# Optimization experiments

Measured on AMD Instinct MI355X. Metric: run time of the kernel, lower is better.

Reference implementation:

```python
import jax, jax.numpy as jnp
import numpy as np

B, S, D, H = 2, 4096, 512, 8
HD = D // H
SCALE = HD ** -0.5


def setup_inputs() -> dict:
    key = jax.random.key(0)
    ks = jax.random.split(key, 11)
    std = D ** -0.5
    return {
        "query": jax.random.normal(ks[0], (B, S, D), jnp.float32),
        "key":   jax.random.normal(ks[1], (B, S, D), jnp.float32),
        "value": jax.random.normal(ks[2], (B, S, D), jnp.float32),
        "wq": jax.random.normal(ks[3], (D, D), jnp.float32) * std,
        "bq": jnp.zeros((D,), jnp.float32),
        "wk": jax.random.normal(ks[4], (D, D), jnp.float32) * std,
        "bk": jnp.zeros((D,), jnp.float32),
        "wv": jax.random.normal(ks[5], (D, D), jnp.float32) * std,
        "bv": jnp.zeros((D,), jnp.float32),
        "wo": jax.random.normal(ks[6], (D, D), jnp.float32) * std,
        "bo": jnp.zeros((D,), jnp.float32),
    }


def reference(query, key, value, wq, bq, wk, bk, wv, bv, wo, bo):
    # projections: [B,S,D] -> [B,H,S,HD]
    def split_heads(x):
        return x.reshape(B, S, H, HD).transpose(0, 2, 1, 3)

    q = split_heads(query @ wq + bq)
    k = split_heads(key @ wk + bk)
    v = split_heads(value @ wv + bv)

    # full O(S^2) score matrix, as in the original naive MHA
    scores = jnp.einsum("bhqd,bhkd->bhqk", q, k) * SCALE  # [B,H,S,S]
    attn_weights = jax.nn.softmax(scores, axis=-1)
    attn_output = jnp.einsum("bhqk,bhkd->bhqd", attn_weights, v)
    attn_output = attn_output.transpose(0, 2, 1, 3).reshape(B, S, D)
    attn_output = attn_output @ wo + bo
    return attn_output, attn_weights
```

## Files before the change

kernel.cpp:

```cpp
#include <hip/hip_runtime.h>
#include <hip/hip_bf16.h>
#include <cstdint>
#include <cstddef>

#define B_  2
#define S_  4096
#define D_  512
#define H_  8
#define HD_ 64
#define QSCALE_ 0.18033688f

typedef short s16x8 __attribute__((ext_vector_type(8)));
typedef float f32x4 __attribute__((ext_vector_type(4)));

__device__ __forceinline__ unsigned short f2bf(float f) {
    unsigned u = __builtin_bit_cast(unsigned, f);
    u += 0x7fffu + ((u >> 16) & 1u);
    return (unsigned short)(u >> 16);
}

__device__ __forceinline__ unsigned packbf2(float a, float b) {
    unsigned r;
    asm("v_cvt_pk_bf16_f32 %0, %1, %2" : "=v"(r) : "v"(a), "v"(b));
    return r;
}

__device__ __forceinline__ void gload16(const unsigned short* g, const unsigned short* l) {
    __builtin_amdgcn_global_load_lds(
        (const __attribute__((address_space(1))) void*)g,
        (__attribute__((address_space(3))) void*)l,
        16, 0, 0);
}

__device__ __forceinline__ s16x8 kfr(const unsigned short* buf, int kr, int hb) {
    return *(const s16x8*)((const char*)buf + kr * 128 + (hb ^ ((kr & 7) << 4)));
}
__device__ __forceinline__ s16x8 vfr_(const unsigned short* buf, int vr, int kbyte) {
    return *(const s16x8*)((const char*)buf + vr * 256 + (kbyte ^ ((vr & 15) << 4)));
}

__global__ __launch_bounds__(256)
void prep_weights(const float* __restrict__ wq, const float* __restrict__ wk,
                  const float* __restrict__ wv, const float* __restrict__ wo,
                  unsigned short* __restrict__ wt) {
    int e = blockIdx.x * 256 + threadIdx.x;
    int mat = e >> 18;
    int i = e & 262143;
    int n = i >> 9, k = i & 511;
    const float* w = (mat == 0) ? wq : (mat == 1) ? wk : (mat == 2) ? wv : wo;
    wt[(size_t)mat * 262144 + n * 512 + k] = f2bf(w[k * 512 + n]);
}

__global__ __launch_bounds__(256)
void qkv_gemm(const float* __restrict__ qx, const float* __restrict__ kx,
              const float* __restrict__ vx, const unsigned short* __restrict__ wtb,
              const float* __restrict__ bqp, const float* __restrict__ bkp,
              const float* __restrict__ bvp,
              unsigned short* __restrict__ qo, unsigned short* __restrict__ ko,
              unsigned short* __restrict__ vo) {
    __shared__ unsigned short xs[64 * 72];
    __shared__ unsigned short wsd[64 * 72];

    const int z = blockIdx.z;
    const float* xin = (z == 0) ? qx : (z == 1) ? kx : vx;
    const unsigned short* wt = wtb + (size_t)z * 262144;
    const float* bias = (z == 0) ? bqp : (z == 1) ? bkp : bvp;
    const float oscale = (z == 0) ? QSCALE_ : 1.0f;

    const int tid  = threadIdx.x;
    const int wave = tid >> 6, lane = tid & 63;
    const int l15 = lane & 15, l4 = lane >> 4;
    const int row0 = blockIdx.x * 64, col0 = blockIdx.y * 64;
    const int sr = tid >> 2, seg = tid & 3;

    f32x4 acc[4] = {};

    for (int kt = 0; kt < 512; kt += 64) {
        {
            const float* x = xin + (size_t)(row0 + sr) * 512 + kt + seg * 16;
            unsigned short tmp[16];
            #pragma unroll
            for (int j = 0; j < 16; j += 4) {
                float4 v = *(const float4*)(x + j);
                tmp[j] = f2bf(v.x); tmp[j+1] = f2bf(v.y); tmp[j+2] = f2bf(v.z); tmp[j+3] = f2bf(v.w);
            }
            *(s16x8*)&xs[sr * 72 + seg * 16]     = *(s16x8*)&tmp[0];
            *(s16x8*)&xs[sr * 72 + seg * 16 + 8] = *(s16x8*)&tmp[8];
        }
        {
            const unsigned short* wp = wt + (size_t)(col0 + sr) * 512 + kt + seg * 16;
            *(s16x8*)&wsd[sr * 72 + seg * 16]     = *(const s16x8*)(wp);
            *(s16x8*)&wsd[sr * 72 + seg * 16 + 8] = *(const s16x8*)(wp + 8);
        }
        __syncthreads();

        #pragma unroll
        for (int ks = 0; ks < 2; ++ks) {
            s16x8 a = *(const s16x8*)&xs[(wave * 16 + l15) * 72 + ks * 32 + l4 * 8];
            #pragma unroll
            for (int ng = 0; ng < 4; ++ng) {
                s16x8 b = *(const s16x8*)&wsd[(ng * 16 + l15) * 72 + ks * 32 + l4 * 8];
                acc[ng] = __builtin_amdgcn_mfma_f32_16x16x32_bf16(a, b, acc[ng], 0, 0, 0);
            }
        }
        __syncthreads();
    }

    if (z == 2) {
        #pragma unroll
        for (int ng = 0; ng < 4; ++ng) {
            float bv = bias[col0 + ng * 16 + l15];
            #pragma unroll
            for (int r = 0; r < 4; ++r)
                xs[(ng * 16 + l15) * 72 + wave * 16 + l4 * 4 + r] = f2bf(acc[ng][r] + bv);
        }
        __syncthreads();
        const int bb = row0 >> 12, s0l = row0 & 4095, hh = col0 >> 6;
        unsigned short* dst = vo + ((size_t)(bb * H_ + hh) * HD_ + sr) * S_ + s0l + seg * 16;
        *(s16x8*)dst       = *(const s16x8*)&xs[sr * 72 + seg * 16];
        *(s16x8*)(dst + 8) = *(const s16x8*)&xs[sr * 72 + seg * 16 + 8];
    } else {
        unsigned short* out = (z == 0) ? qo : ko;
        #pragma unroll
        for (int ng = 0; ng < 4; ++ng) {
            int c = col0 + ng * 16 + l15;
            float bv = bias[c];
            #pragma unroll
            for (int r = 0; r < 4; ++r) {
                int t = row0 + wave * 16 + l4 * 4 + r;
                out[(size_t)t * 512 + c] = f2bf((acc[ng][r] + bv) * oscale);
            }
        }
    }
}

__global__ __launch_bounds__(256)
void oproj_gemm(const unsigned short* __restrict__ xin, const unsigned short* __restrict__ wt,
                const float* __restrict__ bias, float* __restrict__ out) {
    __shared__ unsigned short xs[64 * 72];
    __shared__ unsigned short wsd[64 * 72];

    const int tid  = threadIdx.x;
    const int wave = tid >> 6, lane = tid & 63;
    const int l15 = lane & 15, l4 = lane >> 4;
    const int row0 = blockIdx.x * 64, col0 = blockIdx.y * 64;
    const int sr = tid >> 2, seg = tid & 3;

    f32x4 acc[4] = {};

    for (int kt = 0; kt < 512; kt += 64) {
        {
            const unsigned short* x = xin + (size_t)(row0 + sr) * 512 + kt + seg * 16;
            *(s16x8*)&xs[sr * 72 + seg * 16]     = *(const s16x8*)(x);
            *(s16x8*)&xs[sr * 72 + seg * 16 + 8] = *(const s16x8*)(x + 8);
        }
        {
            const unsigned short* wp = wt + (size_t)(col0 + sr) * 512 + kt + seg * 16;
            *(s16x8*)&wsd[sr * 72 + seg * 16]     = *(const s16x8*)(wp);
            *(s16x8*)&wsd[sr * 72 + seg * 16 + 8] = *(const s16x8*)(wp + 8);
        }
        __syncthreads();

        #pragma unroll
        for (int ks = 0; ks < 2; ++ks) {
            s16x8 a = *(const s16x8*)&xs[(wave * 16 + l15) * 72 + ks * 32 + l4 * 8];
            #pragma unroll
            for (int ng = 0; ng < 4; ++ng) {
                s16x8 b = *(const s16x8*)&wsd[(ng * 16 + l15) * 72 + ks * 32 + l4 * 8];
                acc[ng] = __builtin_amdgcn_mfma_f32_16x16x32_bf16(a, b, acc[ng], 0, 0, 0);
            }
        }
        __syncthreads();
    }

    #pragma unroll
    for (int ng = 0; ng < 4; ++ng) {
        int c = col0 + ng * 16 + l15;
        float bv = bias[c];
        #pragma unroll
        for (int r = 0; r < 4; ++r) {
            int t = row0 + wave * 16 + l4 * 4 + r;
            out[(size_t)t * 512 + c] = acc[ng][r] + bv;
        }
    }
}

__global__ __launch_bounds__(256)
void attn_kernel(const unsigned short* __restrict__ qb,
                 const unsigned short* __restrict__ kb,
                 const unsigned short* __restrict__ vt,
                 float* __restrict__ wout,
                 unsigned short* __restrict__ ob) {
    __shared__ unsigned short smem[40960];

    const int tid  = threadIdx.x;
    const int wave = tid >> 6, lane = tid & 63;
    const int l15 = lane & 15, l4 = lane >> 4;

    const int lid = blockIdx.x;
    const int wid = (lid & 7) * 64 + (lid >> 3);
    const int bh = wid >> 5;
    const int q0 = (wid & 31) * 128;
    const int b = bh >> 3, h = bh & 7;

    const int ksrow = lane >> 3;
    const int kscol = 8 * ((lane & 7) ^ ksrow);
    const unsigned short* kstg0 = kb + (size_t)(b * S_ + wave * 32 + ksrow) * 512 + h * 64 + kscol;
    const unsigned short* kstg1 = kb + (size_t)(b * S_ + wave * 64 + ksrow) * 512 + h * 64 + kscol;
    const int vsrow = lane >> 4;

#define KSTAGE1(c, bsel)                                                        \
    { _Pragma("unroll")                                                         \
      for (int i_ = 0; i_ < 8; ++i_)                                            \
          gload16(kstg1 + ((size_t)(c) * 256 + i_ * 8) * 512,                   \
                  smem + (bsel) * 16384 + (wave * 64 + i_ * 8) * 64); }

#define KSTAGE(c, bsel)                                                         \
    { _Pragma("unroll")                                                         \
      for (int i_ = 0; i_ < 4; ++i_)                                            \
          gload16(kstg0 + ((size_t)(c) * 128 + i_ * 8) * 512,                   \
                  smem + (bsel) * 8192 + (wave * 32 + i_ * 8) * 64); }

#define VSTAGE(c, bsel)                                                         \
    { _Pragma("unroll")                                                         \
      for (int i_ = 0; i_ < 4; ++i_) {                                          \
          int vrow_ = wave * 16 + i_ * 4 + vsrow;                               \
          int vcb_  = (lane & 15) ^ (i_ * 4 + vsrow);                           \
          gload16(vt + ((size_t)(bh * 64) + vrow_) * 4096 + (c) * 128 + vcb_ * 8, \
                  smem + 16384 + (bsel) * 8192 + (wave * 16 + i_ * 4) * 128); } }

    s16x8 aq[2][2];
    #pragma unroll
    for (int qh = 0; qh < 2; ++qh) {
        const int t = b * S_ + q0 + wave * 32 + qh * 16 + l15;
        const unsigned short* qp = qb + (size_t)t * 512 + h * 64;
        aq[qh][0] = *(const s16x8*)(qp + l4 * 8);
        aq[qh][1] = *(const s16x8*)(qp + 32 + l4 * 8);
    }

    float lsum[2] = {0.0f, 0.0f};
    KSTAGE1(0, 0);
    __syncthreads();

    for (int c = 0; c < 16; ++c) {
        const int cur = c & 1;
        if (c < 15) KSTAGE1(c + 1, cur ^ 1);
        const unsigned short* kcur = smem + cur * 16384;

        #pragma unroll
        for (int sub = 0; sub < 4; ++sub) {
            f32x4 sc[4][2] = {};
            __builtin_amdgcn_s_setprio(1);
            #pragma unroll
            for (int ks = 0; ks < 2; ++ks)
                #pragma unroll
                for (int kg = 0; kg < 4; ++kg) {
                    s16x8 kf = kfr(kcur, sub * 64 + kg * 16 + l15, ks * 64 + l4 * 16);
                    sc[kg][0] = __builtin_amdgcn_mfma_f32_16x16x32_bf16(kf, aq[0][ks], sc[kg][0], 0, 0, 0);
                    sc[kg][1] = __builtin_amdgcn_mfma_f32_16x16x32_bf16(kf, aq[1][ks], sc[kg][1], 0, 0, 0);
                }
            __builtin_amdgcn_s_setprio(0);
            #pragma unroll
            for (int kg = 0; kg < 4; ++kg)
                #pragma unroll
                for (int r = 0; r < 4; ++r) {
                    lsum[0] += __builtin_amdgcn_exp2f(sc[kg][0][r]);
                    lsum[1] += __builtin_amdgcn_exp2f(sc[kg][1][r]);
                }
        }
        __syncthreads();
    }

    #pragma unroll
    for (int qh = 0; qh < 2; ++qh) {
        lsum[qh] += __shfl_xor(lsum[qh], 16);
        lsum[qh] += __shfl_xor(lsum[qh], 32);
    }
    const float off[2] = { -__builtin_amdgcn_logf(lsum[0]),
                           -__builtin_amdgcn_logf(lsum[1]) };

    f32x4 ao[2][4] = {};
    float* wbase = wout + ((size_t)bh * S_ + q0 + wave * 32) * S_;
    unsigned short* strip = smem + 32768 + wave * 2048;

    KSTAGE(0, 0); VSTAGE(0, 0);
    __syncthreads();

    for (int c = 0; c < 32; ++c) {
        const int cur = c & 1;
        if (c < 31) { KSTAGE(c + 1, cur ^ 1); VSTAGE(c + 1, cur ^ 1); }
        const unsigned short* kcur = smem + cur * 8192;
        const unsigned short* vcur = smem + 16384 + cur * 8192;

        #pragma unroll
        for (int sub = 0; sub < 2; ++sub) {
            f32x4 sc[4][2] = {};
            __builtin_amdgcn_s_setprio(1);
            #pragma unroll
            for (int ks = 0; ks < 2; ++ks)
                #pragma unroll
                for (int kg = 0; kg < 4; ++kg) {
                    s16x8 kf = kfr(kcur, sub * 64 + kg * 16 + l15, ks * 64 + l4 * 16);
                    sc[kg][0] = __builtin_amdgcn_mfma_f32_16x16x32_bf16(kf, aq[0][ks], sc[kg][0], 0, 0, 0);
                    sc[kg][1] = __builtin_amdgcn_mfma_f32_16x16x32_bf16(kf, aq[1][ks], sc[kg][1], 0, 0, 0);
                }
            __builtin_amdgcn_s_setprio(0);

            #pragma unroll
            for (int qh = 0; qh < 2; ++qh) {
                float* wrow = wbase + (size_t)(qh * 16 + l15) * S_ + c * 128 + sub * 64;
                const int q = qh * 16 + l15;
                #pragma unroll
                for (int kg = 0; kg < 4; ++kg) {
                    f32x4 w;
                    #pragma unroll
                    for (int r = 0; r < 4; ++r)
                        w[r] = __builtin_amdgcn_exp2f(sc[kg][qh][r] + off[qh]);
                    *(f32x4*)(wrow + kg * 16 + l4 * 4) = w;
                    uint2 pk;
                    pk.x = packbf2(w[0], w[1]);
                    pk.y = packbf2(w[2], w[3]);
                    *(uint2*)((char*)strip + q * 128 + ((kg * 32 + l4 * 8) ^ ((q & 7) << 4))) = pk;
                }
            }

            __builtin_amdgcn_s_setprio(1);
            #pragma unroll
            for (int ks = 0; ks < 2; ++ks) {
                s16x8 pa0 = *(const s16x8*)((const char*)strip + l15 * 128
                               + ((ks * 64 + l4 * 16) ^ ((l15 & 7) << 4)));
                s16x8 pa1 = *(const s16x8*)((const char*)strip + (16 + l15) * 128
                               + ((ks * 64 + l4 * 16) ^ ((l15 & 7) << 4)));
                #pragma unroll
                for (int ng = 0; ng < 4; ++ng) {
                    s16x8 vf = vfr_(vcur, ng * 16 + l15, sub * 128 + ks * 64 + l4 * 16);
                    ao[0][ng] = __builtin_amdgcn_mfma_f32_16x16x32_bf16(pa0, vf, ao[0][ng], 0, 0, 0);
                    ao[1][ng] = __builtin_amdgcn_mfma_f32_16x16x32_bf16(pa1, vf, ao[1][ng], 0, 0, 0);
                }
            }
            __builtin_amdgcn_s_setprio(0);
        }
        __syncthreads();
    }

    #pragma unroll
    for (int qg = 0; qg < 2; ++qg)
        #pragma unroll
        for (int ng = 0; ng < 4; ++ng) {
            int hd = ng * 16 + l15;
            #pragma unroll
            for (int r = 0; r < 4; ++r) {
                int t = b * S_ + q0 + wave * 32 + qg * 16 + l4 * 4 + r;
                ob[(size_t)t * 512 + h * 64 + hd] = f2bf(ao[qg][ng][r]);
            }
        }
#undef KSTAGE1
#undef KSTAGE
#undef VSTAGE
}

extern "C" void kernel_launch(void* const* d_in, const int* in_sizes, int n_in,
                              void* d_out, int out_size, void* d_ws, size_t ws_size,
                              hipStream_t stream) {
    (void)in_sizes; (void)n_in; (void)out_size; (void)ws_size;

    const float* query = (const float*)d_in[0];
    const float* key_  = (const float*)d_in[1];
    const float* value = (const float*)d_in[2];
    const float* wq = (const float*)d_in[3];
    const float* bq = (const float*)d_in[4];
    const float* wk = (const float*)d_in[5];
    const float* bk = (const float*)d_in[6];
    const float* wv = (const float*)d_in[7];
    const float* bv = (const float*)d_in[8];
    const float* wo = (const float*)d_in[9];
    const float* bo = (const float*)d_in[10];
    float* out = (float*)d_out;

    char* ws = (char*)d_ws;
    unsigned short* wt = (unsigned short*)(ws);
    unsigned short* qb = (unsigned short*)(ws + 2097152);
    unsigned short* kb = (unsigned short*)(ws + 2097152 + 1 * 8388608);
    unsigned short* vt = (unsigned short*)(ws + 2097152 + 2 * 8388608);
    unsigned short* ob = (unsigned short*)(ws + 2097152 + 3 * 8388608);

    hipLaunchKernelGGL(prep_weights, dim3(4096), dim3(256), 0, stream, wq, wk, wv, wo, wt);

    hipLaunchKernelGGL(qkv_gemm, dim3(128, 8, 3), dim3(256), 0, stream,
                       query, key_, value, wt, bq, bk, bv, qb, kb, vt);

    hipLaunchKernelGGL(attn_kernel, dim3(512), dim3(256), 0, stream,
                       qb, kb, vt, out + 4194304, ob);

    hipLaunchKernelGGL(oproj_gemm, dim3(128, 8), dim3(256), 0, stream,
                       ob, wt + 3 * 262144, bo, out);
}
```

Baseline: 354.7 us.

## Enlarge QKV GEMM tiles to 128x128 with swizzled LDS and async B loads

The QKV projection GEMM moves from 64x64 to 128x128 output tiles, with each of the four waves computing a 64x64 sub-tile of 4x4 MFMA fragments. This raises operand reuse from shared memory and cuts redundant global reads of the activations and weights. Padded LDS rows become XOR-swizzled rows, and weight tiles are loaded with the gload16 direct-to-LDS helper. The V transpose epilogue gets wider vectorised stores. The trade-offs are more accumulator registers and fewer blocks (768 instead of 3072), which may lower occupancy. This kernel is also a small part of total time, which is dominated by attention.

```diff
diff --git a/kernel.cpp b/kernel.cpp
--- a/kernel.cpp
+++ b/kernel.cpp
@@ -58,8 +58,9 @@
               const float* __restrict__ bvp,
               unsigned short* __restrict__ qo, unsigned short* __restrict__ ko,
               unsigned short* __restrict__ vo) {
-    __shared__ unsigned short xs[64 * 72];
-    __shared__ unsigned short wsd[64 * 72];
+    __shared__ unsigned short smem[16384];
+    unsigned short* as_ = smem;
+    unsigned short* bs_ = smem + 8192;
 
     const int z = blockIdx.z;
     const float* xin = (z == 0) ? qx : (z == 1) ? kx : vx;
@@ -70,66 +71,89 @@
     const int tid  = threadIdx.x;
     const int wave = tid >> 6, lane = tid & 63;
     const int l15 = lane & 15, l4 = lane >> 4;
-    const int row0 = blockIdx.x * 64, col0 = blockIdx.y * 64;
-    const int sr = tid >> 2, seg = tid & 3;
-
-    f32x4 acc[4] = {};
+    const int wr = wave >> 1, wc = wave & 1;
+    const int row0 = blockIdx.x * 128, col0 = blockIdx.y * 128;
+
+    const int arow = tid >> 1, ahalf = tid & 1;
+    const float* asrc0 = xin + (size_t)(row0 + arow) * 512 + ahalf * 32;
+
+    const int srow = lane >> 3;
+    const int scol = 8 * ((lane & 7) ^ srow);
+    const unsigned short* bsrc0 = wt + (size_t)(col0 + wave * 32 + srow) * 512 + scol;
+
+    f32x4 acc[4][4] = {};
 
     for (int kt = 0; kt < 512; kt += 64) {
+        #pragma unroll
+        for (int i = 0; i < 4; ++i)
+            gload16(bsrc0 + (size_t)i * 8 * 512 + kt, bs_ + (wave * 32 + i * 8) * 64);
         {
-            const float* x = xin + (size_t)(row0 + sr) * 512 + kt + seg * 16;
-            unsigned short tmp[16];
-            #pragma unroll
-            for (int j = 0; j < 16; j += 4) {
-                float4 v = *(const float4*)(x + j);
-                tmp[j] = f2bf(v.x); tmp[j+1] = f2bf(v.y); tmp[j+2] = f2bf(v.z); tmp[j+3] = f2bf(v.w);
-            }
-            *(s16x8*)&xs[sr * 72 + seg * 16]     = *(s16x8*)&tmp[0];
-            *(s16x8*)&xs[sr * 72 + seg * 16 + 8] = *(s16x8*)&tmp[8];
-        }
-        {
-            const unsigned short* wp = wt + (size_t)(col0 + sr) * 512 + kt + seg * 16;
-            *(s16x8*)&wsd[sr * 72 + seg * 16]     = *(const s16x8*)(wp);
-            *(s16x8*)&wsd[sr * 72 + seg * 16 + 8] = *(const s16x8*)(wp + 8);
+            const float* a = asrc0 + kt;
+            #pragma unroll
+            for (int j = 0; j < 4; ++j) {
+                float4 v0 = *(const float4*)(a + j * 8);
+                float4 v1 = *(const float4*)(a + j * 8 + 4);
+                uint4 pk;
+                pk.x = packbf2(v0.x, v0.y); pk.y = packbf2(v0.z, v0.w);
+                pk.z = packbf2(v1.x, v1.y); pk.w = packbf2(v1.z, v1.w);
+                *(uint4*)((char*)as_ + arow * 128 + ((ahalf * 64 + j * 16) ^ ((arow & 7) << 4))) = pk;
+            }
         }
         __syncthreads();
 
         #pragma unroll
         for (int ks = 0; ks < 2; ++ks) {
-            s16x8 a = *(const s16x8*)&xs[(wave * 16 + l15) * 72 + ks * 32 + l4 * 8];
-            #pragma unroll
-            for (int ng = 0; ng < 4; ++ng) {
-                s16x8 b = *(const s16x8*)&wsd[(ng * 16 + l15) * 72 + ks * 32 + l4 * 8];
-                acc[ng] = __builtin_amdgcn_mfma_f32_16x16x32_bf16(a, b, acc[ng], 0, 0, 0);
-            }
+            s16x8 af[4], bf[4];
+            #pragma unroll
+            for (int i = 0; i < 4; ++i) {
+                af[i] = kfr(as_, wr * 64 + i * 16 + l15, ks * 64 + l4 * 16);
+                bf[i] = kfr(bs_, wc * 64 + i * 16 + l15, ks * 64 + l4 * 16);
+            }
+            #pragma unroll
+            for (int mf = 0; mf < 4; ++mf)
+                #pragma unroll
+                for (int nf = 0; nf < 4; ++nf)
+                    acc[mf][nf] = __builtin_amdgcn_mfma_f32_16x16x32_bf16(af[mf], bf[nf], acc[mf][nf], 0, 0, 0);
         }
         __syncthreads();
     }
 
     if (z == 2) {
         #pragma unroll
-        for (int ng = 0; ng < 4; ++ng) {
-            float bv = bias[col0 + ng * 16 + l15];
-            #pragma unroll
-            for (int r = 0; r < 4; ++r)
-                xs[(ng * 16 + l15) * 72 + wave * 16 + l4 * 4 + r] = f2bf(acc[ng][r] + bv);
-        }
-        __syncthreads();
-        const int bb = row0 >> 12, s0l = row0 & 4095, hh = col0 >> 6;
-        unsigned short* dst = vo + ((size_t)(bb * H_ + hh) * HD_ + sr) * S_ + s0l + seg * 16;
-        *(s16x8*)dst       = *(const s16x8*)&xs[sr * 72 + seg * 16];
-        *(s16x8*)(dst + 8) = *(const s16x8*)&xs[sr * 72 + seg * 16 + 8];
+        for (int nf = 0; nf < 4; ++nf) {
+            const int nl = wc * 64 + nf * 16 + l15;
+            float bv = bias[col0 + nl];
+            #pragma unroll
+            for (int mf = 0; mf < 4; ++mf) {
+                uint2 pk;
+                pk.x = packbf2(acc[mf][nf][0] + bv, acc[mf][nf][1] + bv);
+                pk.y = packbf2(acc[mf][nf][2] + bv, acc[mf][nf][3] + bv);
+                int mb = (wr * 64 + mf * 16 + l4 * 4) * 2;
+                *(uint2*)((char*)smem + nl * 256 + (mb ^ ((nl & 7) << 4))) = pk;
+            }
+        }
+        __syncthreads();
+        const int nl = tid >> 1, half = tid & 1;
+        const int c = col0 + nl, hh = c >> 6, hd = c & 63;
+        const int bb = row0 >> 12, s0 = row0 & 4095;
+        unsigned short* dst = vo + ((size_t)(bb * H_ + hh) * HD_ + hd) * S_ + s0 + half * 64;
+        #pragma unroll
+        for (int u = 0; u < 8; ++u)
+            *(uint4*)((char*)dst + u * 16) =
+                *(const uint4*)((char*)smem + nl * 256 + ((half * 128 + u * 16) ^ ((nl & 7) << 4)));
     } else {
         unsigned short* out = (z == 0) ? qo : ko;
         #pragma unroll
-        for (int ng = 0; ng < 4; ++ng) {
-            int c = col0 + ng * 16 + l15;
+        for (int nf = 0; nf < 4; ++nf) {
+            int c = col0 + wc * 64 + nf * 16 + l15;
             float bv = bias[c];
             #pragma unroll
-            for (int r = 0; r < 4; ++r) {
-                int t = row0 + wave * 16 + l4 * 4 + r;
-                out[(size_t)t * 512 + c] = f2bf((acc[ng][r] + bv) * oscale);
-            }
+            for (int mf = 0; mf < 4; ++mf)
+                #pragma unroll
+                for (int r = 0; r < 4; ++r) {
+                    int t = row0 + wr * 64 + mf * 16 + l4 * 4 + r;
+                    out[(size_t)t * 512 + c] = f2bf((acc[mf][nf][r] + bv) * oscale);
+                }
         }
     }
 }
@@ -386,7 +410,7 @@
 
     hipLaunchKernelGGL(prep_weights, dim3(4096), dim3(256), 0, stream, wq, wk, wv, wo, wt);
 
-    hipLaunchKernelGGL(qkv_gemm, dim3(128, 8, 3), dim3(256), 0, stream,
+    hipLaunchKernelGGL(qkv_gemm, dim3(64, 4, 3), dim3(256), 0, stream,
                        query, key_, value, wt, bq, bk, bv, qb, kb, vt);
 
     hipLaunchKernelGGL(attn_kernel, dim3(512), dim3(256), 0, stream,
```

New measurement: 350.6 us. No clear change (-1.2%).
